# Kernel tuning notes

Hardware: AMD Instinct MI355X
Metric: run time of the kernel (lower is better)

The kernel has to match this reference:

```python
import jax, jax.numpy as jnp
import numpy as np

VOCAB, D, BLOCK = 32000, 1024, 2048
B, S = 4, 2048

def setup_inputs() -> dict:
    key = jax.random.key(0)
    ks = jax.random.split(key, 12)
    s = 0.02
    return {
        "x": jax.random.randint(ks[0], (B, S), 0, VOCAB),
        "tok_emb": jax.random.normal(ks[1], (VOCAB, D), jnp.float32) * s,
        "pos_emb": jax.random.normal(ks[2], (BLOCK, D), jnp.float32) * s,
        "Wq": jax.random.normal(ks[3], (D, D), jnp.float32) * s,
        "bq": jnp.zeros((D,), jnp.float32),
        "Wk": jax.random.normal(ks[4], (D, D), jnp.float32) * s,
        "bk": jnp.zeros((D,), jnp.float32),
        "Wv": jax.random.normal(ks[5], (D, D), jnp.float32) * s,
        "bv": jnp.zeros((D,), jnp.float32),
        "Wfc": jax.random.normal(ks[6], (VOCAB, D), jnp.float32) * s,
        "bfc": jnp.zeros((VOCAB,), jnp.float32),
    }

def reference(x, tok_emb, pos_emb, Wq, bq, Wk, bk, Wv, bv, Wfc, bfc):
    # embeddings: token lookup + learned positional
    h = tok_emb[x] + pos_emb[jnp.arange(x.shape[1])][None, :, :]  # [B,S,D]
    Q = h @ Wq.T + bq
    K = h @ Wk.T + bk
    V = h @ Wv.T + bv
    scale = 1.0 / jnp.sqrt(jnp.float32(Q.shape[-1]))
    scores = jnp.einsum('bqd,bkd->bqk', Q, K) * scale  # [B,S,S]
    attn = jax.nn.softmax(scores, axis=-1)
    out = jnp.einsum('bqk,bkd->bqd', attn, V)
    return out @ Wfc.T + bfc  # [B,S,VOCAB]
```

## Files before the change

### kernel.cpp

```cpp
#include <hip/hip_runtime.h>
#include <hip/hip_bf16.h>
#include <stdint.h>

typedef __bf16 bf16x8 __attribute__((ext_vector_type(8)));
typedef float f32x4 __attribute__((ext_vector_type(4)));
typedef unsigned short u16x8 __attribute__((ext_vector_type(8)));

#define DEVINL static __device__ __forceinline__

DEVINL unsigned short f2bf(float f) {
  unsigned u = __builtin_bit_cast(unsigned, f);
  unsigned r = (u + 0x7FFFu + ((u >> 16) & 1u)) >> 16;
  return (unsigned short)r;
}
DEVINL float bf2f(unsigned short u) {
  return __builtin_bit_cast(float, ((unsigned)u) << 16);
}

DEVINL void gload_lds16(const unsigned short* g, unsigned short* l) {
  __builtin_amdgcn_global_load_lds(
      (const __attribute__((address_space(1))) void*)g,
      (__attribute__((address_space(3))) void*)l, 16, 0, 0);
}

__global__ __launch_bounds__(256) void embed_kernel(
    const int* __restrict__ x, const float* __restrict__ tok,
    const float* __restrict__ pos, unsigned short* __restrict__ hb)
{
  const int bs = blockIdx.x;
  const int s  = bs & 2047;
  const long trow = (long)x[bs] * 1024;
  const int d = threadIdx.x * 4;
  const float4 t = *(const float4*)(tok + trow + d);
  const float4 p = *(const float4*)(pos + (long)s * 1024 + d);
  ushort4 o;
  o.x = f2bf(t.x + p.x);
  o.y = f2bf(t.y + p.y);
  o.z = f2bf(t.z + p.z);
  o.w = f2bf(t.w + p.w);
  *(ushort4*)(hb + (long)bs * 1024 + d) = o;
}

__global__ __launch_bounds__(256) void cvt_kernel(
    const float* __restrict__ in, unsigned short* __restrict__ out, int n4)
{
  for (int i = blockIdx.x * blockDim.x + threadIdx.x; i < n4;
       i += gridDim.x * blockDim.x) {
    float4 v = ((const float4*)in)[i];
    ushort4 o;
    o.x = f2bf(v.x); o.y = f2bf(v.y); o.z = f2bf(v.z); o.w = f2bf(v.w);
    ((ushort4*)out)[i] = o;
  }
}

template<int OUTMODE>
__global__ __launch_bounds__(256) void gemm_bt(
    const unsigned short* __restrict__ A, const unsigned short* __restrict__ B,
    void* __restrict__ Cout, const float* __restrict__ bias,
    float scale, int M, int N, int K,
    long sA, long sB, long sC, int Mb, long tStride)
{
  __shared__ __align__(16) unsigned short lA[128 * 32];
  __shared__ __align__(16) unsigned short lB[128 * 32];
  const int tid = threadIdx.x, wid = tid >> 6, lane = tid & 63;
  A += (long)blockIdx.z * sA;
  B += (long)blockIdx.z * sB;
  const int bm = blockIdx.y * 128, bn = blockIdx.x * 128;

  const int c0 = wid * 64 + lane, c1 = c0 + 256;
  const unsigned short* gA0 = A + (long)(bm + (c0 >> 2)) * K + (c0 & 3) * 8;
  const unsigned short* gA1 = A + (long)(bm + (c1 >> 2)) * K + (c1 & 3) * 8;
  const unsigned short* gB0 = B + (long)(bn + (c0 >> 2)) * K + (c0 & 3) * 8;
  const unsigned short* gB1 = B + (long)(bn + (c1 >> 2)) * K + (c1 & 3) * 8;
  unsigned short* lA0 = lA + wid * 512;
  unsigned short* lA1 = lA + 2048 + wid * 512;
  unsigned short* lB0 = lB + wid * 512;
  unsigned short* lB1 = lB + 2048 + wid * 512;

  const int wr = (wid >> 1) * 64, wc = (wid & 1) * 64;
  const int lr = lane & 15, lk = (lane >> 4) * 8;

  f32x4 acc[4][4] = {};
  const int nk = K >> 5;
  for (int kt = 0; kt < nk; ++kt) {
    const int ko = kt << 5;
    gload_lds16(gA0 + ko, lA0);
    gload_lds16(gA1 + ko, lA1);
    gload_lds16(gB0 + ko, lB0);
    gload_lds16(gB1 + ko, lB1);
    __syncthreads();
    bf16x8 af[4], bg[4];
#pragma unroll
    for (int m = 0; m < 4; ++m)
      af[m] = *(const bf16x8*)(const void*)(lA + (wr + m * 16 + lr) * 32 + lk);
#pragma unroll
    for (int n = 0; n < 4; ++n)
      bg[n] = *(const bf16x8*)(const void*)(lB + (wc + n * 16 + lr) * 32 + lk);
#pragma unroll
    for (int m = 0; m < 4; ++m)
#pragma unroll
      for (int n = 0; n < 4; ++n)
        acc[m][n] = __builtin_amdgcn_mfma_f32_16x16x32_bf16(af[m], bg[n],
                                                            acc[m][n], 0, 0, 0);
    __syncthreads();
  }

  const int r0 = bm + wr + ((lane >> 4) << 2);
  const int cbase = bn + wc + lr;
#pragma unroll
  for (int n = 0; n < 4; ++n) {
    const int col = cbase + n * 16;
    const float bv = bias ? bias[col] : 0.f;
#pragma unroll
    for (int m = 0; m < 4; ++m) {
      const int row0 = r0 + m * 16;
      if (OUTMODE == 2) {
        float* C = (float*)Cout + (long)blockIdx.z * sC;
#pragma unroll
        for (int i = 0; i < 4; ++i)
          C[(long)(row0 + i) * N + col] = acc[m][n][i] * scale + bv;
      } else if (OUTMODE == 0) {
        unsigned short* C = (unsigned short*)Cout + (long)blockIdx.z * sC;
#pragma unroll
        for (int i = 0; i < 4; ++i)
          C[(long)(row0 + i) * N + col] = f2bf(acc[m][n][i] * scale + bv);
      } else {
        unsigned short* C = (unsigned short*)Cout;
        const int b = row0 / Mb;
        const int srow = row0 - b * Mb;
        ushort4 o;
        o.x = f2bf(acc[m][n][0] * scale + bv);
        o.y = f2bf(acc[m][n][1] * scale + bv);
        o.z = f2bf(acc[m][n][2] * scale + bv);
        o.w = f2bf(acc[m][n][3] * scale + bv);
        *(ushort4*)(C + (long)b * tStride + (long)col * Mb + srow) = o;
      }
    }
  }
}

__global__ __launch_bounds__(256) void qkv_bt(
    const unsigned short* __restrict__ A, const unsigned short* __restrict__ B,
    unsigned short* __restrict__ Qb, unsigned short* __restrict__ Kb,
    unsigned short* __restrict__ Vt,
    const float* __restrict__ bq, const float* __restrict__ bk,
    const float* __restrict__ bv)
{
  constexpr int K = 1024;
  __shared__ __align__(16) unsigned short lA[128 * 32];
  __shared__ __align__(16) unsigned short lB[128 * 32];
  const int tid = threadIdx.x, wid = tid >> 6, lane = tid & 63;
  const int bm = blockIdx.y * 128, bn = blockIdx.x * 128;
  const int sector = bn >> 10;
  const int bnl = bn & 1023;

  const int c0 = wid * 64 + lane, c1 = c0 + 256;
  const unsigned short* gA0 = A + (long)(bm + (c0 >> 2)) * K + (c0 & 3) * 8;
  const unsigned short* gA1 = A + (long)(bm + (c1 >> 2)) * K + (c1 & 3) * 8;
  const unsigned short* gB0 = B + (long)(bn + (c0 >> 2)) * K + (c0 & 3) * 8;
  const unsigned short* gB1 = B + (long)(bn + (c1 >> 2)) * K + (c1 & 3) * 8;
  unsigned short* lA0 = lA + wid * 512;
  unsigned short* lA1 = lA + 2048 + wid * 512;
  unsigned short* lB0 = lB + wid * 512;
  unsigned short* lB1 = lB + 2048 + wid * 512;

  const int wr = (wid >> 1) * 64, wc = (wid & 1) * 64;
  const int lr = lane & 15, lk = (lane >> 4) * 8;

  f32x4 acc[4][4] = {};
  for (int kt = 0; kt < 32; ++kt) {
    const int ko = kt << 5;
    gload_lds16(gA0 + ko, lA0);
    gload_lds16(gA1 + ko, lA1);
    gload_lds16(gB0 + ko, lB0);
    gload_lds16(gB1 + ko, lB1);
    __syncthreads();
    bf16x8 af[4], bg[4];
#pragma unroll
    for (int m = 0; m < 4; ++m)
      af[m] = *(const bf16x8*)(const void*)(lA + (wr + m * 16 + lr) * 32 + lk);
#pragma unroll
    for (int n = 0; n < 4; ++n)
      bg[n] = *(const bf16x8*)(const void*)(lB + (wc + n * 16 + lr) * 32 + lk);
#pragma unroll
    for (int m = 0; m < 4; ++m)
#pragma unroll
      for (int n = 0; n < 4; ++n)
        acc[m][n] = __builtin_amdgcn_mfma_f32_16x16x32_bf16(af[m], bg[n],
                                                            acc[m][n], 0, 0, 0);
    __syncthreads();
  }

  const float* bias = (sector == 0) ? bq : (sector == 1) ? bk : bv;
  const int r0 = bm + wr + ((lane >> 4) << 2);
  const int cbase = bnl + wc + lr;
#pragma unroll
  for (int n = 0; n < 4; ++n) {
    const int col = cbase + n * 16;
    const float bb = bias[col];
#pragma unroll
    for (int m = 0; m < 4; ++m) {
      const int row0 = r0 + m * 16;
      if (sector == 2) {
        const int b = row0 >> 11;
        const int srow = row0 & 2047;
        ushort4 o;
        o.x = f2bf(acc[m][n][0] + bb);
        o.y = f2bf(acc[m][n][1] + bb);
        o.z = f2bf(acc[m][n][2] + bb);
        o.w = f2bf(acc[m][n][3] + bb);
        *(ushort4*)(Vt + (long)b * (1024L * 2048) + (long)col * 2048 + srow) = o;
      } else {
        unsigned short* C = (sector == 0) ? Qb : Kb;
#pragma unroll
        for (int i = 0; i < 4; ++i)
          C[(long)(row0 + i) * 1024 + col] = f2bf(acc[m][n][i] + bb);
      }
    }
  }
}

__global__ __launch_bounds__(256) void softmax_kernel(unsigned short* __restrict__ S)
{
  unsigned short* row = S + (long)blockIdx.x * 2048;
  const int t = threadIdx.x, lane = t & 63, wid = t >> 6;
  __shared__ float redm[4], reds[4];
  u16x8 raw = ((const u16x8*)row)[t];
  float v[8];
#pragma unroll
  for (int j = 0; j < 8; ++j) v[j] = bf2f(raw[j]);
  float mx = v[0];
#pragma unroll
  for (int j = 1; j < 8; ++j) mx = fmaxf(mx, v[j]);
#pragma unroll
  for (int off = 32; off; off >>= 1) mx = fmaxf(mx, __shfl_xor(mx, off, 64));
  if (lane == 0) redm[wid] = mx;
  __syncthreads();
  mx = fmaxf(fmaxf(redm[0], redm[1]), fmaxf(redm[2], redm[3]));
  float s = 0.f;
#pragma unroll
  for (int j = 0; j < 8; ++j) { v[j] = __expf(v[j] - mx); s += v[j]; }
#pragma unroll
  for (int off = 32; off; off >>= 1) s += __shfl_xor(s, off, 64);
  if (lane == 0) reds[wid] = s;
  __syncthreads();
  s = reds[0] + reds[1] + reds[2] + reds[3];
  const float inv = 1.f / s;
  u16x8 o;
#pragma unroll
  for (int j = 0; j < 8; ++j) o[j] = f2bf(v[j] * inv);
  ((u16x8*)row)[t] = o;
}

DEVINL bf16x8 ldfrag(const unsigned short* p, int row, int kx) {
  return *(const bf16x8*)((const char*)p + row * 128 + kx);
}

#define BARSB() do { __builtin_amdgcn_s_barrier(); \
                     __builtin_amdgcn_sched_barrier(0); } while (0)
#define LGK0() asm volatile("s_waitcnt lgkmcnt(0)")
#define VM6()  asm volatile("s_waitcnt vmcnt(6)")

#define MF16(rb, aArr, bArr) do { \
  _Pragma("unroll") for (int m_ = 0; m_ < 4; ++m_) \
  _Pragma("unroll") for (int n_ = 0; n_ < 4; ++n_) \
    acc[(rb) + m_][n_] = __builtin_amdgcn_mfma_f32_16x16x32_bf16( \
        aArr[m_], bArr[n_], acc[(rb) + m_][n_], 0, 0, 0); \
} while (0)

#define STG_A(b, h, gk) do { \
  const char* s_ = srcA + (h) * 262144 + (long)(((gk) & 15)) * 128; \
  gload_lds16((const unsigned short*)(s_ + la0), \
              dA + (b) * 16384 + (h) * 8192 + dO0); \
  gload_lds16((const unsigned short*)(s_ + la1), \
              dA + (b) * 16384 + (h) * 8192 + dO1); } while (0)
#define STG_B(b, h, gk) do { \
  int t_ = (gk) >> 4; if (t_ >= len) t_ = len - 1; \
  const char* s_ = Bbase + ((long)(bnStart + t_) << 19) + \
                   (h) * 262144 + (long)(((gk) & 15)) * 128; \
  gload_lds16((const unsigned short*)(s_ + la0), \
              dB + (b) * 16384 + (h) * 8192 + dO0); \
  gload_lds16((const unsigned short*)(s_ + la1), \
              dB + (b) * 16384 + (h) * 8192 + dO1); } while (0)

#define KTILE(BUF, S1, S2, S3, S4) do { \
  bf16x8 b0_[4], b1_[4], aA_[4], aB_[4], aC_[4], aD_[4]; \
  _Pragma("unroll") for (int n = 0; n < 4; ++n) { \
    b0_[n] = ldfrag(dB + (BUF) * 16384, wn * 64 + n * 16 + lr, kx0); \
    b1_[n] = ldfrag(dB + (BUF) * 16384, wn * 64 + n * 16 + lr, kx1); } \
  _Pragma("unroll") for (int m = 0; m < 4; ++m) \
    aA_[m] = ldfrag(dA + (BUF) * 16384, wm * 128 + m * 16 + lr, kx0); \
  S1; \
  BARSB(); LGK0(); __builtin_amdgcn_s_setprio(1); \
  MF16(0, aA_, b0_); \
  __builtin_amdgcn_s_setprio(0); BARSB(); \
  _Pragma("unroll") for (int m = 0; m < 4; ++m) { \
    aB_[m] = ldfrag(dA + (BUF) * 16384, wm * 128 + (4 + m) * 16 + lr, kx0); \
    aC_[m] = ldfrag(dA + (BUF) * 16384, wm * 128 + (4 + m) * 16 + lr, kx1); } \
  S2; \
  BARSB(); LGK0(); __builtin_amdgcn_s_setprio(1); \
  MF16(4, aB_, b0_); \
  __builtin_amdgcn_s_setprio(0); BARSB(); \
  _Pragma("unroll") for (int m = 0; m < 4; ++m) \
    aD_[m] = ldfrag(dA + (BUF) * 16384, wm * 128 + m * 16 + lr, kx1); \
  S3; \
  BARSB(); LGK0(); __builtin_amdgcn_s_setprio(1); \
  MF16(4, aC_, b1_); \
  __builtin_amdgcn_s_setprio(0); BARSB(); \
  S4; VM6(); \
  BARSB(); LGK0(); __builtin_amdgcn_s_setprio(1); \
  MF16(0, aD_, b1_); \
  __builtin_amdgcn_s_setprio(0); BARSB(); \
} while (0)

__global__ __launch_bounds__(512, 2) void gemm256_fc(
    const unsigned short* __restrict__ A, const unsigned short* __restrict__ B,
    float* __restrict__ C, const float* __restrict__ bias)
{
  constexpr int N = 32000;
  __shared__ __align__(16) unsigned short lds[65536];
  const int tid = threadIdx.x, wid = tid >> 6, lane = tid & 63;
  const int wm = wid >> 2, wn = wid & 3;
  const int lr = lane & 15;
  const int kq = (lane >> 4) << 4;
  const int xr = (lane & 7) << 4;
  const int kx0 = kq ^ xr;
  const int kx1 = (64 | kq) ^ xr;

  const int bid = blockIdx.x;
  const int g = bid & 7;
  const int j = bid >> 3;
  const int bm = g * 4 + (j & 3);
  const int q = j >> 2;
  const int bnStart = (q < 5) ? 16 * q : 80 + (q - 5) * 15;
  const int len = (q < 5) ? 16 : 15;

  const int loff0 = wid * 1024 + lane * 16;
  const int loff1 = loff0 + 8192;
  const int r0 = loff0 >> 7, r1 = loff1 >> 7;
  const int c0 = (loff0 & 127) ^ ((r0 & 7) << 4);
  const int c1 = (loff1 & 127) ^ ((r1 & 7) << 4);
  const long la0 = (long)r0 * 2048 + c0;
  const long la1 = (long)r1 * 2048 + c1;
  const char* srcA = (const char*)A + ((long)bm << 19);
  const char* Bbase = (const char*)B;
  unsigned short* dA = lds;
  unsigned short* dB = lds + 32768;
  const int dO0 = wid * 512, dO1 = 4096 + wid * 512;

  f32x4 acc[8][4] = {};
  float bv[4];
#pragma unroll
  for (int n = 0; n < 4; ++n)
    bv[n] = bias[(long)bnStart * 256 + wn * 64 + n * 16 + lr];

  STG_B(0, 0, 0); STG_B(0, 1, 0); STG_A(0, 0, 0); STG_A(0, 1, 0);
  STG_B(1, 0, 1); STG_B(1, 1, 1); STG_A(1, 0, 1);
  VM6();
  BARSB();

  for (int t = 0; t < len; ++t) {
#pragma unroll 1
    for (int it = 0; it < 8; ++it) {
      const int gk = t * 16 + 2 * it;
      KTILE(0, STG_A(1, 1, gk + 1), STG_B(0, 0, gk + 2), STG_B(0, 1, gk + 2),
            STG_A(0, 0, gk + 2));
      KTILE(1, STG_A(0, 1, gk + 2), STG_B(1, 0, gk + 3), STG_B(1, 1, gk + 3),
            STG_A(1, 0, gk + 3));
    }
    const long bnRow = ((long)bnStart + t) * 256;
    const int q4 = (lane >> 4) * 4;
#pragma unroll
    for (int m = 0; m < 8; ++m) {
      const long row = (long)bm * 256 + wm * 128 + m * 16 + q4;
#pragma unroll
      for (int i = 0; i < 4; ++i) {
        float* orow = C + (row + i) * (long)N;
#pragma unroll
        for (int n = 0; n < 4; ++n)
          __builtin_nontemporal_store(acc[m][n][i] + bv[n],
                                      &orow[bnRow + wn * 64 + n * 16 + lr]);
      }
    }
    VM6();
    const int tn = (t + 1 < len) ? t + 1 : t;
#pragma unroll
    for (int n = 0; n < 4; ++n)
      bv[n] = bias[((long)bnStart + tn) * 256 + wn * 64 + n * 16 + lr];
#pragma unroll
    for (int m = 0; m < 8; ++m)
#pragma unroll
      for (int n = 0; n < 4; ++n)
        acc[m][n] = f32x4{0.f, 0.f, 0.f, 0.f};
  }
}

extern "C" void kernel_launch(void* const* d_in, const int* in_sizes, int n_in,
                              void* d_out, int out_size, void* d_ws, size_t ws_size,
                              hipStream_t stream)
{
  const int*   x   = (const int*)d_in[0];
  const float* tok = (const float*)d_in[1];
  const float* pos = (const float*)d_in[2];
  const float* Wq  = (const float*)d_in[3];
  const float* bq  = (const float*)d_in[4];
  const float* Wk  = (const float*)d_in[5];
  const float* bk  = (const float*)d_in[6];
  const float* Wv  = (const float*)d_in[7];
  const float* bv  = (const float*)d_in[8];
  const float* Wfc = (const float*)d_in[9];
  const float* bfc = (const float*)d_in[10];
  float* out = (float*)d_out;

  char* ws = (char*)d_ws;
  unsigned short* hb   = (unsigned short*)(ws);
  unsigned short* Wqb  = (unsigned short*)(ws + 16777216);
  unsigned short* Wkb  = (unsigned short*)(ws + 18874368);
  unsigned short* Wvb  = (unsigned short*)(ws + 20971520);
  unsigned short* Wfcb = (unsigned short*)(ws + 23068672);
  unsigned short* Qb   = (unsigned short*)(ws + 88604672);
  unsigned short* Kb   = (unsigned short*)(ws + 105381888);
  unsigned short* Vt   = (unsigned short*)(ws + 122159104);
  unsigned short* Sc   = (unsigned short*)(ws + 138936320);
  unsigned short* AO   = hb;

  embed_kernel<<<8192, 256, 0, stream>>>(x, tok, pos, hb);
  cvt_kernel<<<512, 256, 0, stream>>>(Wq, Wqb, 1024 * 1024 / 4);
  cvt_kernel<<<512, 256, 0, stream>>>(Wk, Wkb, 1024 * 1024 / 4);
  cvt_kernel<<<512, 256, 0, stream>>>(Wv, Wvb, 1024 * 1024 / 4);
  cvt_kernel<<<2048, 256, 0, stream>>>(Wfc, Wfcb, 32000 * 1024 / 4);

  dim3 blk(256);
  qkv_bt<<<dim3(24, 64), blk, 0, stream>>>(hb, Wqb, Qb, Kb, Vt, bq, bk, bv);
  gemm_bt<0><<<dim3(16, 16, 4), blk, 0, stream>>>(Qb, Kb, Sc, nullptr, 0.03125f,
      2048, 2048, 1024, 2048L * 1024, 2048L * 1024, 2048L * 2048, 0, 0);
  softmax_kernel<<<8192, 256, 0, stream>>>(Sc);
  gemm_bt<0><<<dim3(8, 16, 4), blk, 0, stream>>>(Sc, Vt, AO, nullptr, 1.f,
      2048, 1024, 2048, 2048L * 2048, 1024L * 2048, 2048L * 1024, 0, 0);
  gemm256_fc<<<dim3(256), dim3(512), 0, stream>>>(AO, Wfcb, out, bfc);
}
```

Baseline: 771.8 us.

## Remap GEMM block indices for XCD-local L2 reuse and fuse weight conversions

The QKV, QK^T and PV GEMMs now launch as 1D grids. Each block index is remapped so that blocks with the same bid&7 (likely the same XCD under round-robin dispatch) work on neighbouring tiles that share A rows or batches. The aim is better L2 reuse of operand tiles on each die. The four weight fp32-to-bf16 conversion launches are also merged into one kernel that writes a contiguous buffer. This removes launch overhead, at the cost of a per-element branch to select the source.

```diff
diff --git a/kernel.cpp b/kernel.cpp
--- a/kernel.cpp
+++ b/kernel.cpp
@@ -41,12 +41,20 @@
   *(ushort4*)(hb + (long)bs * 1024 + d) = o;
 }
 
-__global__ __launch_bounds__(256) void cvt_kernel(
-    const float* __restrict__ in, unsigned short* __restrict__ out, int n4)
-{
-  for (int i = blockIdx.x * blockDim.x + threadIdx.x; i < n4;
-       i += gridDim.x * blockDim.x) {
-    float4 v = ((const float4*)in)[i];
+__global__ __launch_bounds__(256) void cvt4_kernel(
+    const float* __restrict__ wq, const float* __restrict__ wk,
+    const float* __restrict__ wv, const float* __restrict__ wfc,
+    unsigned short* __restrict__ out)
+{
+  for (long i = blockIdx.x * blockDim.x + threadIdx.x; i < 8978432;
+       i += (long)gridDim.x * blockDim.x) {
+    const float* src;
+    long off;
+    if (i < 262144)       { src = wq;  off = i; }
+    else if (i < 524288)  { src = wk;  off = i - 262144; }
+    else if (i < 786432)  { src = wv;  off = i - 524288; }
+    else                  { src = wfc; off = i - 786432; }
+    float4 v = ((const float4*)src)[off];
     ushort4 o;
     o.x = f2bf(v.x); o.y = f2bf(v.y); o.z = f2bf(v.z); o.w = f2bf(v.w);
     ((ushort4*)out)[i] = o;
@@ -58,14 +66,24 @@
     const unsigned short* __restrict__ A, const unsigned short* __restrict__ B,
     void* __restrict__ Cout, const float* __restrict__ bias,
     float scale, int M, int N, int K,
-    long sA, long sB, long sC, int Mb, long tStride)
+    long sA, long sB, long sC, int Mb, long tStride, int mapMode)
 {
   __shared__ __align__(16) unsigned short lA[128 * 32];
   __shared__ __align__(16) unsigned short lB[128 * 32];
   const int tid = threadIdx.x, wid = tid >> 6, lane = tid & 63;
-  A += (long)blockIdx.z * sA;
-  B += (long)blockIdx.z * sB;
-  const int bm = blockIdx.y * 128, bn = blockIdx.x * 128;
+  int bx, by, bz;
+  if (mapMode == 0) {
+    bx = blockIdx.x; by = blockIdx.y; bz = blockIdx.z;
+  } else {
+    const int bid = blockIdx.x;
+    const int g = bid & 7, jj = bid >> 3;
+    bz = g >> 1;
+    by = (g & 1) * 8 + (jj & 7);
+    bx = jj >> 3;
+  }
+  A += (long)bz * sA;
+  B += (long)bz * sB;
+  const int bm = by * 128, bn = bx * 128;
 
   const int c0 = wid * 64 + lane, c1 = c0 + 256;
   const unsigned short* gA0 = A + (long)(bm + (c0 >> 2)) * K + (c0 & 3) * 8;
@@ -115,12 +133,12 @@
     for (int m = 0; m < 4; ++m) {
       const int row0 = r0 + m * 16;
       if (OUTMODE == 2) {
-        float* C = (float*)Cout + (long)blockIdx.z * sC;
+        float* C = (float*)Cout + (long)bz * sC;
 #pragma unroll
         for (int i = 0; i < 4; ++i)
           C[(long)(row0 + i) * N + col] = acc[m][n][i] * scale + bv;
       } else if (OUTMODE == 0) {
-        unsigned short* C = (unsigned short*)Cout + (long)blockIdx.z * sC;
+        unsigned short* C = (unsigned short*)Cout + (long)bz * sC;
 #pragma unroll
         for (int i = 0; i < 4; ++i)
           C[(long)(row0 + i) * N + col] = f2bf(acc[m][n][i] * scale + bv);
@@ -150,7 +168,10 @@
   __shared__ __align__(16) unsigned short lA[128 * 32];
   __shared__ __align__(16) unsigned short lB[128 * 32];
   const int tid = threadIdx.x, wid = tid >> 6, lane = tid & 63;
-  const int bm = blockIdx.y * 128, bn = blockIdx.x * 128;
+  const int bid = blockIdx.x;
+  const int g = bid & 7, j = bid >> 3;
+  const int bm = (g * 8 + (j & 7)) * 128;
+  const int bn = (j >> 3) * 128;
   const int sector = bn >> 10;
   const int bnl = bn & 1023;
 
@@ -415,8 +436,6 @@
   char* ws = (char*)d_ws;
   unsigned short* hb   = (unsigned short*)(ws);
   unsigned short* Wqb  = (unsigned short*)(ws + 16777216);
-  unsigned short* Wkb  = (unsigned short*)(ws + 18874368);
-  unsigned short* Wvb  = (unsigned short*)(ws + 20971520);
   unsigned short* Wfcb = (unsigned short*)(ws + 23068672);
   unsigned short* Qb   = (unsigned short*)(ws + 88604672);
   unsigned short* Kb   = (unsigned short*)(ws + 105381888);
@@ -425,17 +444,14 @@
   unsigned short* AO   = hb;
 
   embed_kernel<<<8192, 256, 0, stream>>>(x, tok, pos, hb);
-  cvt_kernel<<<512, 256, 0, stream>>>(Wq, Wqb, 1024 * 1024 / 4);
-  cvt_kernel<<<512, 256, 0, stream>>>(Wk, Wkb, 1024 * 1024 / 4);
-  cvt_kernel<<<512, 256, 0, stream>>>(Wv, Wvb, 1024 * 1024 / 4);
-  cvt_kernel<<<2048, 256, 0, stream>>>(Wfc, Wfcb, 32000 * 1024 / 4);
+  cvt4_kernel<<<2048, 256, 0, stream>>>(Wq, Wk, Wv, Wfc, Wqb);
 
   dim3 blk(256);
-  qkv_bt<<<dim3(24, 64), blk, 0, stream>>>(hb, Wqb, Qb, Kb, Vt, bq, bk, bv);
-  gemm_bt<0><<<dim3(16, 16, 4), blk, 0, stream>>>(Qb, Kb, Sc, nullptr, 0.03125f,
-      2048, 2048, 1024, 2048L * 1024, 2048L * 1024, 2048L * 2048, 0, 0);
+  qkv_bt<<<dim3(1536), blk, 0, stream>>>(hb, Wqb, Qb, Kb, Vt, bq, bk, bv);
+  gemm_bt<0><<<dim3(1024), blk, 0, stream>>>(Qb, Kb, Sc, nullptr, 0.03125f,
+      2048, 2048, 1024, 2048L * 1024, 2048L * 1024, 2048L * 2048, 0, 0, 1);
   softmax_kernel<<<8192, 256, 0, stream>>>(Sc);
-  gemm_bt<0><<<dim3(8, 16, 4), blk, 0, stream>>>(Sc, Vt, AO, nullptr, 1.f,
-      2048, 1024, 2048, 2048L * 2048, 1024L * 2048, 2048L * 1024, 0, 0);
+  gemm_bt<0><<<dim3(512), blk, 0, stream>>>(Sc, Vt, AO, nullptr, 1.f,
+      2048, 1024, 2048, 2048L * 2048, 1024L * 2048, 2048L * 1024, 0, 0, 1);
   gemm256_fc<<<dim3(256), dim3(512), 0, stream>>>(AO, Wfcb, out, bfc);
 }
```

Result: no change. 774.0 us (+0.3%).
